# Kernel tuning notes

Hardware: AMD Instinct MI355X
Metric: run time of the kernel (lower is better)

Reference implementation:

```python
import jax, jax.numpy as jnp
import numpy as np

H_HEADS = 16
N_HID = 1024
D_K = N_HID // H_HEADS
EPS = 1e-6


def _linear(x, w, b):
    # torch nn.Linear: y = x @ W^T + b, W is [out, in]
    return jnp.einsum('bsi,oi->bso', x, w) + b


def _layernorm(x, a, b):
    # Faithful to custom LayerNorm: unbiased std (torch default) and (std + eps)
    mean = jnp.mean(x, axis=-1, keepdims=True)
    std = jnp.std(x, axis=-1, keepdims=True, ddof=1)
    return a * (x - mean) / (std + EPS) + b


def setup_inputs() -> dict:
    key = jax.random.key(0)
    ks = jax.random.split(key, 20)
    B, S, H = 4, 1024, N_HID
    s = 1.0 / np.sqrt(H)
    inp = {
        'x': jax.random.normal(ks[0], (B, S, H), dtype=jnp.float32),
        'mask': jax.random.randint(ks[1], (B, 1, 1, S), 0, 2, dtype=jnp.int32),
        'wq': jax.random.normal(ks[2], (H, H), dtype=jnp.float32) * s,
        'bq': jnp.zeros((H,), jnp.float32),
        'wk': jax.random.normal(ks[3], (H, H), dtype=jnp.float32) * s,
        'bk': jnp.zeros((H,), jnp.float32),
        'wv': jax.random.normal(ks[4], (H, H), dtype=jnp.float32) * s,
        'bv': jnp.zeros((H,), jnp.float32),
        'wo': jax.random.normal(ks[5], (H, H), dtype=jnp.float32) * s,
        'bo': jnp.zeros((H,), jnp.float32),
        'w1': jax.random.normal(ks[6], (2 * H, H), dtype=jnp.float32) * s,
        'b1': jnp.zeros((2 * H,), jnp.float32),
        'w2': jax.random.normal(ks[7], (H, 2 * H), dtype=jnp.float32) * (1.0 / np.sqrt(2 * H)),
        'b2': jnp.zeros((H,), jnp.float32),
        'g1': jnp.ones((H,), jnp.float32),
        'be1': jnp.zeros((H,), jnp.float32),
        'g2': jnp.ones((H,), jnp.float32),
        'be2': jnp.zeros((H,), jnp.float32),
    }
    return inp


def _forward(x, mask, wq, bq, wk, bk, wv, bv, wo, bo, w1, b1, w2, b2, g1, be1, g2, be2):
    B, S, H = x.shape
    # --- multi-head self-attention ---
    q = _linear(x, wq, bq).reshape(B, S, H_HEADS, D_K).transpose(0, 2, 1, 3)  # [B,h,S,dk]
    k = _linear(x, wk, bk).reshape(B, S, H_HEADS, D_K).transpose(0, 2, 1, 3)
    v = _linear(x, wv, bv).reshape(B, S, H_HEADS, D_K).transpose(0, 2, 1, 3)
    scores = jnp.einsum('bhqd,bhkd->bhqk', q, k) / np.sqrt(D_K)  # [B,h,S,S]
    scores = jnp.where(mask == 0, jnp.float32(-1e9), scores)
    p = jax.nn.softmax(scores, axis=-1)
    attn_out = jnp.einsum('bhqk,bhkd->bhqd', p, v)
    attn_out = attn_out.transpose(0, 2, 1, 3).reshape(B, S, H)
    attn_out = _linear(attn_out, wo, bo)
    # sublayer 0: residual + layernorm (dropout = identity at eval)
    x = _layernorm(x + attn_out, g1, be1)
    # --- positionwise FFN ---
    ff = _linear(jax.nn.relu(_linear(x, w1, b1)), w2, b2)
    # sublayer 1
    return _layernorm(x + ff, g2, be2)


def reference(x, mask, wq, bq, wk, bk, wv, bv, wo, bo, w1, b1, w2, b2, g1, be1, g2, be2):
    return _forward(x, mask, wq, bq, wk, bk, wv, bv, wo, bo, w1, b1, w2, b2, g1, be1, g2, be2)
```

## Files before the change

### kernel.cpp

```cpp
#include <hip/hip_runtime.h>

typedef __attribute__((ext_vector_type(8))) short short8;
typedef __attribute__((ext_vector_type(4))) float f32x4;
typedef __attribute__((ext_vector_type(4))) unsigned short us4;

#define LOG2E 1.4426950408889634f

__device__ __forceinline__ unsigned short f2bf(float f) {
  unsigned int u = __float_as_uint(f);
  u += 0x7FFFu + ((u >> 16) & 1u);
  return (unsigned short)(u >> 16);
}

__global__ __launch_bounds__(256) void cvt_all(
    const float* __restrict__ x, const float* __restrict__ wq, const float* __restrict__ wk,
    const float* __restrict__ wv, const float* __restrict__ wo, const float* __restrict__ w1,
    const float* __restrict__ w2,
    unsigned short* __restrict__ xb, unsigned short* __restrict__ wqkvb,
    unsigned short* __restrict__ wob, unsigned short* __restrict__ w1b,
    unsigned short* __restrict__ w2b) {
  int i = blockIdx.x * 256 + threadIdx.x;
  for (int t = i; t < 3145728; t += 786432) {
    const float* src; unsigned short* dst; int lo;
    if (t < 1048576)      { src = x;  dst = xb;              lo = t; }
    else if (t < 1310720) { src = wq; dst = wqkvb;           lo = t - 1048576; }
    else if (t < 1572864) { src = wk; dst = wqkvb + 1048576; lo = t - 1310720; }
    else if (t < 1835008) { src = wv; dst = wqkvb + 2097152; lo = t - 1572864; }
    else if (t < 2097152) { src = wo; dst = wob;             lo = t - 1835008; }
    else if (t < 2621440) { src = w1; dst = w1b;             lo = t - 2097152; }
    else                  { src = w2; dst = w2b;             lo = t - 2621440; }
    float4 v = ((const float4*)src)[lo];
    us4 o = { f2bf(v.x), f2bf(v.y), f2bf(v.z), f2bf(v.w) };
    *(us4*)(dst + (size_t)lo * 4) = o;
  }
}

#define GLL16(g, l) __builtin_amdgcn_global_load_lds( \
    (const __attribute__((address_space(1))) void*)(g), \
    (__attribute__((address_space(3))) void*)(l), 16, 0, 0)

template <int EPI>
__global__ __launch_bounds__(256) void gemm_bt(
    const unsigned short* __restrict__ A, const unsigned short* __restrict__ B,
    const float* __restrict__ bias, const float* __restrict__ res,
    void* __restrict__ out, int M, int N, int K) {
  __shared__ __align__(16) unsigned short As[128 * 64];
  __shared__ __align__(16) unsigned short Bs[128 * 64];
  const int tid = threadIdx.x;
  const int lane = tid & 63;
  const int w = tid >> 6;
  const int wr = w >> 1, wc = w & 1;
  const int l15 = lane & 15, l4 = lane >> 4;
  const int m0 = blockIdx.y * 128, n0 = blockIdx.x * 128;

  f32x4 acc[4][4] = {};

  const int nkt = K >> 6;
  for (int kt = 0; kt < nkt; ++kt) {
    __syncthreads();
#pragma unroll
    for (int i = 0; i < 4; ++i) {
      int c = (i * 4 + w) * 64 + lane;
      int row = c >> 3;
      int offb = (c & 7) * 16;
      int srcb = offb ^ ((row & 7) << 4);
      const unsigned short* ga = A + (size_t)(m0 + row) * K + kt * 64 + (srcb >> 1);
      GLL16(ga, As + (i * 4 + w) * 512);
      const unsigned short* gb = B + (size_t)(n0 + row) * K + kt * 64 + (srcb >> 1);
      GLL16(gb, Bs + (i * 4 + w) * 512);
    }
    __syncthreads();
#pragma unroll
    for (int ks = 0; ks < 2; ++ks) {
      short8 a[4], b[4];
#pragma unroll
      for (int mi = 0; mi < 4; ++mi) {
        int row = wr * 64 + mi * 16 + l15;
        int ke = (ks * 32 + l4 * 8) ^ ((row & 7) << 3);
        a[mi] = *(const short8*)(As + row * 64 + ke);
      }
#pragma unroll
      for (int ni = 0; ni < 4; ++ni) {
        int row = wc * 64 + ni * 16 + l15;
        int ke = (ks * 32 + l4 * 8) ^ ((row & 7) << 3);
        b[ni] = *(const short8*)(Bs + row * 64 + ke);
      }
#pragma unroll
      for (int mi = 0; mi < 4; ++mi)
#pragma unroll
        for (int ni = 0; ni < 4; ++ni)
          acc[mi][ni] = __builtin_amdgcn_mfma_f32_16x16x32_bf16(a[mi], b[ni], acc[mi][ni], 0, 0, 0);
    }
  }

#pragma unroll
  for (int mi = 0; mi < 4; ++mi) {
#pragma unroll
    for (int ni = 0; ni < 4; ++ni) {
      int n = n0 + wc * 64 + ni * 16 + l15;
      float bv = bias[n];
#pragma unroll
      for (int j = 0; j < 4; ++j) {
        int m = m0 + wr * 64 + mi * 16 + l4 * 4 + j;
        float v = acc[mi][ni][j] + bv;
        if (EPI == 0) {
          ((float*)out)[(size_t)m * N + n] = v + res[(size_t)m * N + n];
        } else {
          ((unsigned short*)out)[(size_t)m * N + n] = f2bf(v > 0.f ? v : 0.f);
        }
      }
    }
  }
}

template <int EPI>
__global__ __launch_bounds__(256) void gemm_bt64(
    const unsigned short* __restrict__ A, const unsigned short* __restrict__ B,
    const float* __restrict__ bias, const float* __restrict__ res,
    void* __restrict__ out, int M, int N, int K) {
  __shared__ __align__(16) unsigned short As[128 * 64];
  __shared__ __align__(16) unsigned short Bs[64 * 64];
  const int tid = threadIdx.x;
  const int lane = tid & 63;
  const int w = tid >> 6;
  const int l15 = lane & 15, l4 = lane >> 4;
  const int m0 = blockIdx.y * 128, n0 = blockIdx.x * 64;

  f32x4 acc[2][4] = {};

  const int nkt = K >> 6;
  for (int kt = 0; kt < nkt; ++kt) {
    __syncthreads();
#pragma unroll
    for (int i = 0; i < 4; ++i) {
      int chunk = i * 4 + w;
      int c = chunk * 64 + lane;
      int row = c >> 3;
      int offb = (c & 7) * 16;
      int srcb = offb ^ ((row & 7) << 4);
      GLL16(A + (size_t)(m0 + row) * K + kt * 64 + (srcb >> 1), As + chunk * 512);
    }
#pragma unroll
    for (int i = 0; i < 2; ++i) {
      int chunk = i * 4 + w;
      int c = chunk * 64 + lane;
      int row = c >> 3;
      int offb = (c & 7) * 16;
      int srcb = offb ^ ((row & 7) << 4);
      GLL16(B + (size_t)(n0 + row) * K + kt * 64 + (srcb >> 1), Bs + chunk * 512);
    }
    __syncthreads();
#pragma unroll
    for (int ks = 0; ks < 2; ++ks) {
      short8 a[2], b[4];
#pragma unroll
      for (int mi = 0; mi < 2; ++mi) {
        int row = w * 32 + mi * 16 + l15;
        int ke = (ks * 32 + l4 * 8) ^ ((row & 7) << 3);
        a[mi] = *(const short8*)(As + row * 64 + ke);
      }
#pragma unroll
      for (int ni = 0; ni < 4; ++ni) {
        int row = ni * 16 + l15;
        int ke = (ks * 32 + l4 * 8) ^ ((row & 7) << 3);
        b[ni] = *(const short8*)(Bs + row * 64 + ke);
      }
#pragma unroll
      for (int mi = 0; mi < 2; ++mi)
#pragma unroll
        for (int ni = 0; ni < 4; ++ni)
          acc[mi][ni] = __builtin_amdgcn_mfma_f32_16x16x32_bf16(a[mi], b[ni], acc[mi][ni], 0, 0, 0);
    }
  }

#pragma unroll
  for (int mi = 0; mi < 2; ++mi) {
#pragma unroll
    for (int ni = 0; ni < 4; ++ni) {
      int n = n0 + ni * 16 + l15;
      float bv = bias[n];
#pragma unroll
      for (int j = 0; j < 4; ++j) {
        int m = m0 + w * 32 + mi * 16 + l4 * 4 + j;
        float v = acc[mi][ni][j] + bv;
        if (EPI == 0) {
          ((float*)out)[(size_t)m * N + n] = v + res[(size_t)m * N + n];
        } else {
          ((unsigned short*)out)[(size_t)m * N + n] = f2bf(v > 0.f ? v : 0.f);
        }
      }
    }
  }
}

__global__ __launch_bounds__(256) void gemm_qkv(
    const unsigned short* __restrict__ A,
    const unsigned short* __restrict__ Bw,
    const float* __restrict__ bq, const float* __restrict__ bk, const float* __restrict__ bvv,
    unsigned short* __restrict__ Qo, unsigned short* __restrict__ Ko, unsigned short* __restrict__ Vto,
    int K) {
  __shared__ __align__(16) unsigned short As[128 * 64];
  __shared__ __align__(16) unsigned short Bs[128 * 64];
  const int tid = threadIdx.x;
  const int lane = tid & 63;
  const int w = tid >> 6;
  const int wr = w >> 1, wc = w & 1;
  const int l15 = lane & 15, l4 = lane >> 4;
  const int m0 = blockIdx.y * 128, n0 = blockIdx.x * 128;
  const bool swp = (n0 >= 2048);

  f32x4 acc[4][4] = {};

  const int nkt = K >> 6;
  for (int kt = 0; kt < nkt; ++kt) {
    __syncthreads();
#pragma unroll
    for (int i = 0; i < 4; ++i) {
      int c = (i * 4 + w) * 64 + lane;
      int row = c >> 3;
      int offb = (c & 7) * 16;
      int srcb = offb ^ ((row & 7) << 4);
      GLL16(A + (size_t)(m0 + row) * K + kt * 64 + (srcb >> 1), As + (i * 4 + w) * 512);
      GLL16(Bw + (size_t)(n0 + row) * K + kt * 64 + (srcb >> 1), Bs + (i * 4 + w) * 512);
    }
    __syncthreads();
#pragma unroll
    for (int ks = 0; ks < 2; ++ks) {
      short8 a[4], b[4];
#pragma unroll
      for (int mi = 0; mi < 4; ++mi) {
        int row = wr * 64 + mi * 16 + l15;
        int ke = (ks * 32 + l4 * 8) ^ ((row & 7) << 3);
        a[mi] = *(const short8*)(As + row * 64 + ke);
      }
#pragma unroll
      for (int ni = 0; ni < 4; ++ni) {
        int row = wc * 64 + ni * 16 + l15;
        int ke = (ks * 32 + l4 * 8) ^ ((row & 7) << 3);
        b[ni] = *(const short8*)(Bs + row * 64 + ke);
      }
      if (!swp) {
#pragma unroll
        for (int mi = 0; mi < 4; ++mi)
#pragma unroll
          for (int ni = 0; ni < 4; ++ni)
            acc[mi][ni] = __builtin_amdgcn_mfma_f32_16x16x32_bf16(a[mi], b[ni], acc[mi][ni], 0, 0, 0);
      } else {
#pragma unroll
        for (int mi = 0; mi < 4; ++mi)
#pragma unroll
          for (int ni = 0; ni < 4; ++ni)
            acc[mi][ni] = __builtin_amdgcn_mfma_f32_16x16x32_bf16(b[ni], a[mi], acc[mi][ni], 0, 0, 0);
      }
    }
  }

  if (!swp) {
#pragma unroll
    for (int mi = 0; mi < 4; ++mi) {
#pragma unroll
      for (int ni = 0; ni < 4; ++ni) {
        int n = n0 + wc * 64 + ni * 16 + l15;
        int seg = n >> 10;
        int nn = n & 1023;
        int h_ = nn >> 6, d_ = nn & 63;
        float bval = (seg == 0 ? bq : bk)[nn];
#pragma unroll
        for (int j = 0; j < 4; ++j) {
          int m = m0 + wr * 64 + mi * 16 + l4 * 4 + j;
          int b_ = m >> 10, s_ = m & 1023;
          float v = acc[mi][ni][j] + bval;
          size_t headbase = ((size_t)(b_ * 16 + h_)) << 16;
          if (seg == 0) Qo[headbase + (s_ << 6) + d_] = f2bf(v * 0.125f);
          else          Ko[headbase + (s_ << 6) + d_] = f2bf(v);
        }
      }
    }
  } else {
#pragma unroll
    for (int ni = 0; ni < 4; ++ni) {
      float bval[4];
      int nbase = (n0 & 1023) + wc * 64 + ni * 16 + l4 * 4;
#pragma unroll
      for (int j = 0; j < 4; ++j) bval[j] = bvv[nbase + j];
#pragma unroll
      for (int mi = 0; mi < 4; ++mi) {
        int m = m0 + wr * 64 + mi * 16 + l15;
        int b_ = m >> 10, s_ = m & 1023;
#pragma unroll
        for (int j = 0; j < 4; ++j) {
          int nn = nbase + j;
          int h_ = nn >> 6, d_ = nn & 63;
          float v = acc[mi][ni][j] + bval[j];
          Vto[(((size_t)(b_ * 16 + h_)) << 16) + (d_ << 10) + s_] = f2bf(v);
        }
      }
    }
  }
}

__global__ __launch_bounds__(256) void attn_kernel(
    const unsigned short* __restrict__ Qg, const unsigned short* __restrict__ Kg,
    const unsigned short* __restrict__ Vtg, const int* __restrict__ mask,
    unsigned short* __restrict__ Og) {
  __shared__ __align__(16) unsigned short Qs[64 * 64];
  __shared__ __align__(16) unsigned short Ks[64 * 64];
  __shared__ __align__(16) unsigned short Vs[64 * 64];
  __shared__ __align__(16) unsigned short Ps[4][16 * 64];
  __shared__ float mkadd[1024];

  const int tid = threadIdx.x, lane = tid & 63, w = tid >> 6;
  const int l15 = lane & 15, l4 = lane >> 4;
  const int bh = blockIdx.y;
  const int b = bh >> 4, h = bh & 15;
  const int s0 = blockIdx.x * 64;

  const unsigned short* Qbase = Qg + ((size_t)bh << 16);
  const unsigned short* Kbase = Kg + ((size_t)bh << 16);
  const unsigned short* Vbase = Vtg + ((size_t)bh << 16);

#pragma unroll
  for (int i = 0; i < 4; ++i)
    mkadd[i * 256 + tid] = (mask[b * 1024 + i * 256 + tid] == 0) ? -1e9f : 0.f;

#pragma unroll
  for (int i = 0; i < 2; ++i) {
    int c = i * 256 + tid;
    int row = c >> 3, off8 = (c & 7) * 8;
    short8 v = *(const short8*)(Qbase + (size_t)(s0 + row) * 64 + off8);
    *(short8*)(&Qs[row * 64 + (off8 ^ ((row & 7) << 3))]) = v;
  }

  f32x4 o[4] = {};
  float l_st[4] = {0.f, 0.f, 0.f, 0.f};

  for (int kv = 0; kv < 16; ++kv) {
    int kv0 = kv * 64;
    __syncthreads();
#pragma unroll
    for (int i = 0; i < 2; ++i) {
      int c = i * 256 + tid;
      int row = c >> 3, off8 = (c & 7) * 8;
      short8 kvv = *(const short8*)(Kbase + (size_t)(kv0 + row) * 64 + off8);
      *(short8*)(&Ks[row * 64 + (off8 ^ ((row & 7) << 3))]) = kvv;
      short8 vv = *(const short8*)(Vbase + (size_t)row * 1024 + kv0 + off8);
      *(short8*)(&Vs[row * 64 + (off8 ^ ((row & 7) << 3))]) = vv;
    }
    __syncthreads();

    f32x4 sc[4] = {};
#pragma unroll
    for (int ks = 0; ks < 2; ++ks) {
      short8 a, bb[4];
      {
        int row = w * 16 + l15;
        int ke = (ks * 32 + l4 * 8) ^ ((row & 7) << 3);
        a = *(const short8*)(Qs + row * 64 + ke);
      }
#pragma unroll
      for (int ni = 0; ni < 4; ++ni) {
        int row = ni * 16 + l15;
        int ke = (ks * 32 + l4 * 8) ^ ((row & 7) << 3);
        bb[ni] = *(const short8*)(Ks + row * 64 + ke);
      }
#pragma unroll
      for (int ni = 0; ni < 4; ++ni)
        sc[ni] = __builtin_amdgcn_mfma_f32_16x16x32_bf16(a, bb[ni], sc[ni], 0, 0, 0);
    }

#pragma unroll
    for (int j = 0; j < 4; ++j) {
      int r = l4 * 4 + j;
      float ps = 0.f;
#pragma unroll
      for (int ni = 0; ni < 4; ++ni) {
        int cc = ni * 16 + l15;
        float p = exp2f(fmaf(sc[ni][j], LOG2E, mkadd[kv0 + cc]));
        ps += p;
        Ps[w][r * 64 + (cc ^ ((r & 7) << 3))] = f2bf(p);
      }
      l_st[j] += ps;
    }

#pragma unroll
    for (int ks = 0; ks < 2; ++ks) {
      short8 a, bb[4];
      {
        int row = l15;
        int ke = (ks * 32 + l4 * 8) ^ ((row & 7) << 3);
        a = *(const short8*)(&Ps[w][row * 64 + ke]);
      }
#pragma unroll
      for (int dt = 0; dt < 4; ++dt) {
        int row = dt * 16 + l15;
        int ke = (ks * 32 + l4 * 8) ^ ((row & 7) << 3);
        bb[dt] = *(const short8*)(Vs + row * 64 + ke);
      }
#pragma unroll
      for (int dt = 0; dt < 4; ++dt)
        o[dt] = __builtin_amdgcn_mfma_f32_16x16x32_bf16(a, bb[dt], o[dt], 0, 0, 0);
    }
  }

#pragma unroll
  for (int j = 0; j < 4; ++j) {
#pragma unroll
    for (int off = 1; off < 16; off <<= 1) l_st[j] += __shfl_xor(l_st[j], off, 64);
  }

#pragma unroll
  for (int j = 0; j < 4; ++j) {
    float inv = 1.f / l_st[j];
    int s = s0 + w * 16 + l4 * 4 + j;
#pragma unroll
    for (int dt = 0; dt < 4; ++dt) {
      int d = dt * 16 + l15;
      Og[(((size_t)(b * 1024 + s)) << 10) + h * 64 + d] = f2bf(o[dt][j] * inv);
    }
  }
}

template <int WRITE_BF16>
__global__ __launch_bounds__(256) void ln_kernel(
    const float* __restrict__ z, const float* __restrict__ g, const float* __restrict__ be,
    float* __restrict__ outf, unsigned short* __restrict__ outb) {
  int row = blockIdx.x * 4 + (threadIdx.x >> 6);
  int lane = threadIdx.x & 63;
  const float4* zp = (const float4*)(z + (size_t)row * 1024);
  float4 v[4];
  float sum = 0.f, sq = 0.f;
#pragma unroll
  for (int k = 0; k < 4; ++k) {
    v[k] = zp[lane + k * 64];
    sum += v[k].x + v[k].y + v[k].z + v[k].w;
    sq += v[k].x * v[k].x + v[k].y * v[k].y + v[k].z * v[k].z + v[k].w * v[k].w;
  }
#pragma unroll
  for (int off = 1; off < 64; off <<= 1) {
    sum += __shfl_xor(sum, off, 64);
    sq += __shfl_xor(sq, off, 64);
  }
  float mean = sum * (1.f / 1024.f);
  float var = fmaxf((sq - sum * mean) * (1.f / 1023.f), 0.f);
  float r = 1.f / (sqrtf(var) + 1e-6f);
#pragma unroll
  for (int k = 0; k < 4; ++k) {
    int c = lane + k * 64;
    float4 gv = ((const float4*)g)[c];
    float4 bv = ((const float4*)be)[c];
    float4 y;
    y.x = (v[k].x - mean) * r * gv.x + bv.x;
    y.y = (v[k].y - mean) * r * gv.y + bv.y;
    y.z = (v[k].z - mean) * r * gv.z + bv.z;
    y.w = (v[k].w - mean) * r * gv.w + bv.w;
    ((float4*)(outf + (size_t)row * 1024))[c] = y;
    if (WRITE_BF16) {
      us4 ob = { f2bf(y.x), f2bf(y.y), f2bf(y.z), f2bf(y.w) };
      *(us4*)(outb + (size_t)row * 1024 + c * 4) = ob;
    }
  }
}

extern "C" void kernel_launch(void* const* d_in, const int* in_sizes, int n_in,
                              void* d_out, int out_size, void* d_ws, size_t ws_size,
                              hipStream_t stream) {
  (void)in_sizes; (void)n_in; (void)out_size; (void)ws_size;
  const float* x   = (const float*)d_in[0];
  const int*   msk = (const int*)d_in[1];
  const float* wq  = (const float*)d_in[2];
  const float* bq  = (const float*)d_in[3];
  const float* wk  = (const float*)d_in[4];
  const float* bk  = (const float*)d_in[5];
  const float* wv  = (const float*)d_in[6];
  const float* bv  = (const float*)d_in[7];
  const float* wo  = (const float*)d_in[8];
  const float* bo  = (const float*)d_in[9];
  const float* w1  = (const float*)d_in[10];
  const float* b1  = (const float*)d_in[11];
  const float* w2  = (const float*)d_in[12];
  const float* b2  = (const float*)d_in[13];
  const float* g1  = (const float*)d_in[14];
  const float* be1 = (const float*)d_in[15];
  const float* g2  = (const float*)d_in[16];
  const float* be2 = (const float*)d_in[17];
  float* out = (float*)d_out;

  char* ws = (char*)d_ws;
  const size_t MB = 1 << 20;
  unsigned short* xb    = (unsigned short*)(ws + 0 * MB);
  unsigned short* wqkvb = (unsigned short*)(ws + 8 * MB);
  unsigned short* wob   = (unsigned short*)(ws + 14 * MB);
  unsigned short* w1b   = (unsigned short*)(ws + 16 * MB);
  unsigned short* w2b   = (unsigned short*)(ws + 20 * MB);
  unsigned short* Qb    = (unsigned short*)(ws + 24 * MB);
  unsigned short* Kb    = (unsigned short*)(ws + 32 * MB);
  unsigned short* Vtb   = (unsigned short*)(ws + 40 * MB);
  unsigned short* attnb = (unsigned short*)(ws + 48 * MB);
  float* z1   = (float*)(ws + 56 * MB);
  float* x1f  = (float*)(ws + 72 * MB);
  unsigned short* x1b = (unsigned short*)(ws + 88 * MB);
  unsigned short* h1  = (unsigned short*)(ws + 24 * MB);
  float* z2 = (float*)(ws + 56 * MB);

  dim3 blk(256);

  cvt_all<<<3072, blk, 0, stream>>>(x, wq, wk, wv, wo, w1, w2, xb, wqkvb, wob, w1b, w2b);

  gemm_qkv<<<dim3(24, 32), blk, 0, stream>>>(xb, wqkvb, bq, bk, bv, Qb, Kb, Vtb, 1024);

  attn_kernel<<<dim3(16, 64), blk, 0, stream>>>(Qb, Kb, Vtb, msk, attnb);

  gemm_bt64<0><<<dim3(16, 32), blk, 0, stream>>>(attnb, wob, bo, x, (void*)z1, 4096, 1024, 1024);
  ln_kernel<1><<<1024, blk, 0, stream>>>(z1, g1, be1, x1f, x1b);

  gemm_bt<3><<<dim3(16, 32), blk, 0, stream>>>(x1b, w1b, b1, nullptr, (void*)h1, 4096, 2048, 1024);
  gemm_bt64<0><<<dim3(16, 32), blk, 0, stream>>>(h1, w2b, b2, x1f, (void*)z2, 4096, 1024, 2048);
  ln_kernel<0><<<1024, blk, 0, stream>>>(z2, g2, be2, out, nullptr);
}
```

Baseline: 193.6 us.

## Double-buffer LDS tiles in GEMMs and shrink QKV tile to 128x64

The GEMM kernels now use two LDS buffers and issue the global-to-LDS loads for the next K tile before computing on the current one, with a single barrier per iteration instead of two. The separate 128- and 64-wide GEMM kernels are merged into one template. The QKV projection switches from 128x128 to 128x64 tiles, doubling its grid to raise occupancy and wave count. The cost is doubled LDS per block, which may reduce how many blocks fit per CU.

After: 183.2 us. 5.4% less time.

```diff
diff --git a/kernel.cpp b/kernel.cpp
--- a/kernel.cpp
+++ b/kernel.cpp
@@ -39,69 +39,83 @@
     (const __attribute__((address_space(1))) void*)(g), \
     (__attribute__((address_space(3))) void*)(l), 16, 0, 0)
 
-template <int EPI>
-__global__ __launch_bounds__(256) void gemm_bt(
+template <int BN, int EPI>
+__global__ __launch_bounds__(256) void gemm2(
     const unsigned short* __restrict__ A, const unsigned short* __restrict__ B,
     const float* __restrict__ bias, const float* __restrict__ res,
     void* __restrict__ out, int M, int N, int K) {
-  __shared__ __align__(16) unsigned short As[128 * 64];
-  __shared__ __align__(16) unsigned short Bs[128 * 64];
+  __shared__ __align__(16) unsigned short As[2][128 * 64];
+  __shared__ __align__(16) unsigned short Bs[2][BN * 64];
   const int tid = threadIdx.x;
   const int lane = tid & 63;
   const int w = tid >> 6;
-  const int wr = w >> 1, wc = w & 1;
   const int l15 = lane & 15, l4 = lane >> 4;
-  const int m0 = blockIdx.y * 128, n0 = blockIdx.x * 128;
-
-  f32x4 acc[4][4] = {};
+  const int m0 = blockIdx.y * 128, n0 = blockIdx.x * BN;
+
+  constexpr int MI = (BN == 128) ? 4 : 2;
+  f32x4 acc[MI][4] = {};
+
+  auto STAGE = [&](int buf, int kt) {
+#pragma unroll
+    for (int i = 0; i < 4; ++i) {
+      int chunk = i * 4 + w;
+      int c = chunk * 64 + lane;
+      int row = c >> 3;
+      int srcb = ((c & 7) * 16) ^ ((row & 7) << 4);
+      GLL16(A + (size_t)(m0 + row) * K + kt * 64 + (srcb >> 1), &As[buf][chunk * 512]);
+    }
+#pragma unroll
+    for (int i = 0; i < BN / 32; ++i) {
+      int chunk = i * 4 + w;
+      int c = chunk * 64 + lane;
+      int row = c >> 3;
+      int srcb = ((c & 7) * 16) ^ ((row & 7) << 4);
+      GLL16(B + (size_t)(n0 + row) * K + kt * 64 + (srcb >> 1), &Bs[buf][chunk * 512]);
+    }
+  };
 
   const int nkt = K >> 6;
+  STAGE(0, 0);
+  __syncthreads();
+  int cur = 0;
   for (int kt = 0; kt < nkt; ++kt) {
-    __syncthreads();
-#pragma unroll
-    for (int i = 0; i < 4; ++i) {
-      int c = (i * 4 + w) * 64 + lane;
-      int row = c >> 3;
-      int offb = (c & 7) * 16;
-      int srcb = offb ^ ((row & 7) << 4);
-      const unsigned short* ga = A + (size_t)(m0 + row) * K + kt * 64 + (srcb >> 1);
-      GLL16(ga, As + (i * 4 + w) * 512);
-      const unsigned short* gb = B + (size_t)(n0 + row) * K + kt * 64 + (srcb >> 1);
-      GLL16(gb, Bs + (i * 4 + w) * 512);
-    }
-    __syncthreads();
+    if (kt + 1 < nkt) STAGE(cur ^ 1, kt + 1);
+    const unsigned short* as = As[cur];
+    const unsigned short* bs = Bs[cur];
 #pragma unroll
     for (int ks = 0; ks < 2; ++ks) {
-      short8 a[4], b[4];
-#pragma unroll
-      for (int mi = 0; mi < 4; ++mi) {
-        int row = wr * 64 + mi * 16 + l15;
-        int ke = (ks * 32 + l4 * 8) ^ ((row & 7) << 3);
-        a[mi] = *(const short8*)(As + row * 64 + ke);
+      short8 a[MI], b[4];
+#pragma unroll
+      for (int mi = 0; mi < MI; ++mi) {
+        int row = (BN == 128 ? ((w >> 1) * 64) : (w * 32)) + mi * 16 + l15;
+        int ke = (ks * 32 + l4 * 8) ^ ((row & 7) << 3);
+        a[mi] = *(const short8*)(as + row * 64 + ke);
       }
 #pragma unroll
       for (int ni = 0; ni < 4; ++ni) {
-        int row = wc * 64 + ni * 16 + l15;
-        int ke = (ks * 32 + l4 * 8) ^ ((row & 7) << 3);
-        b[ni] = *(const short8*)(Bs + row * 64 + ke);
-      }
-#pragma unroll
-      for (int mi = 0; mi < 4; ++mi)
+        int row = (BN == 128 ? ((w & 1) * 64) : 0) + ni * 16 + l15;
+        int ke = (ks * 32 + l4 * 8) ^ ((row & 7) << 3);
+        b[ni] = *(const short8*)(bs + row * 64 + ke);
+      }
+#pragma unroll
+      for (int mi = 0; mi < MI; ++mi)
 #pragma unroll
         for (int ni = 0; ni < 4; ++ni)
           acc[mi][ni] = __builtin_amdgcn_mfma_f32_16x16x32_bf16(a[mi], b[ni], acc[mi][ni], 0, 0, 0);
     }
-  }
-
-#pragma unroll
-  for (int mi = 0; mi < 4; ++mi) {
+    __syncthreads();
+    cur ^= 1;
+  }
+
+#pragma unroll
+  for (int mi = 0; mi < MI; ++mi) {
 #pragma unroll
     for (int ni = 0; ni < 4; ++ni) {
-      int n = n0 + wc * 64 + ni * 16 + l15;
+      int n = n0 + (BN == 128 ? ((w & 1) * 64) : 0) + ni * 16 + l15;
       float bv = bias[n];
 #pragma unroll
       for (int j = 0; j < 4; ++j) {
-        int m = m0 + wr * 64 + mi * 16 + l4 * 4 + j;
+        int m = m0 + (BN == 128 ? ((w >> 1) * 64) : (w * 32)) + mi * 16 + l4 * 4 + j;
         float v = acc[mi][ni][j] + bv;
         if (EPI == 0) {
           ((float*)out)[(size_t)m * N + n] = v + res[(size_t)m * N + n];
@@ -113,161 +127,96 @@
   }
 }
 
-template <int EPI>
-__global__ __launch_bounds__(256) void gemm_bt64(
-    const unsigned short* __restrict__ A, const unsigned short* __restrict__ B,
-    const float* __restrict__ bias, const float* __restrict__ res,
-    void* __restrict__ out, int M, int N, int K) {
-  __shared__ __align__(16) unsigned short As[128 * 64];
-  __shared__ __align__(16) unsigned short Bs[64 * 64];
-  const int tid = threadIdx.x;
-  const int lane = tid & 63;
-  const int w = tid >> 6;
-  const int l15 = lane & 15, l4 = lane >> 4;
-  const int m0 = blockIdx.y * 128, n0 = blockIdx.x * 64;
-
-  f32x4 acc[2][4] = {};
-
-  const int nkt = K >> 6;
-  for (int kt = 0; kt < nkt; ++kt) {
-    __syncthreads();
-#pragma unroll
-    for (int i = 0; i < 4; ++i) {
-      int chunk = i * 4 + w;
-      int c = chunk * 64 + lane;
-      int row = c >> 3;
-      int offb = (c & 7) * 16;
-      int srcb = offb ^ ((row & 7) << 4);
-      GLL16(A + (size_t)(m0 + row) * K + kt * 64 + (srcb >> 1), As + chunk * 512);
-    }
-#pragma unroll
-    for (int i = 0; i < 2; ++i) {
-      int chunk = i * 4 + w;
-      int c = chunk * 64 + lane;
-      int row = c >> 3;
-      int offb = (c & 7) * 16;
-      int srcb = offb ^ ((row & 7) << 4);
-      GLL16(B + (size_t)(n0 + row) * K + kt * 64 + (srcb >> 1), Bs + chunk * 512);
-    }
-    __syncthreads();
-#pragma unroll
-    for (int ks = 0; ks < 2; ++ks) {
-      short8 a[2], b[4];
-#pragma unroll
-      for (int mi = 0; mi < 2; ++mi) {
-        int row = w * 32 + mi * 16 + l15;
-        int ke = (ks * 32 + l4 * 8) ^ ((row & 7) << 3);
-        a[mi] = *(const short8*)(As + row * 64 + ke);
-      }
-#pragma unroll
-      for (int ni = 0; ni < 4; ++ni) {
-        int row = ni * 16 + l15;
-        int ke = (ks * 32 + l4 * 8) ^ ((row & 7) << 3);
-        b[ni] = *(const short8*)(Bs + row * 64 + ke);
-      }
-#pragma unroll
-      for (int mi = 0; mi < 2; ++mi)
-#pragma unroll
-        for (int ni = 0; ni < 4; ++ni)
-          acc[mi][ni] = __builtin_amdgcn_mfma_f32_16x16x32_bf16(a[mi], b[ni], acc[mi][ni], 0, 0, 0);
-    }
-  }
-
-#pragma unroll
-  for (int mi = 0; mi < 2; ++mi) {
-#pragma unroll
-    for (int ni = 0; ni < 4; ++ni) {
-      int n = n0 + ni * 16 + l15;
-      float bv = bias[n];
-#pragma unroll
-      for (int j = 0; j < 4; ++j) {
-        int m = m0 + w * 32 + mi * 16 + l4 * 4 + j;
-        float v = acc[mi][ni][j] + bv;
-        if (EPI == 0) {
-          ((float*)out)[(size_t)m * N + n] = v + res[(size_t)m * N + n];
-        } else {
-          ((unsigned short*)out)[(size_t)m * N + n] = f2bf(v > 0.f ? v : 0.f);
-        }
-      }
-    }
-  }
-}
-
 __global__ __launch_bounds__(256) void gemm_qkv(
     const unsigned short* __restrict__ A,
     const unsigned short* __restrict__ Bw,
     const float* __restrict__ bq, const float* __restrict__ bk, const float* __restrict__ bvv,
     unsigned short* __restrict__ Qo, unsigned short* __restrict__ Ko, unsigned short* __restrict__ Vto,
     int K) {
-  __shared__ __align__(16) unsigned short As[128 * 64];
-  __shared__ __align__(16) unsigned short Bs[128 * 64];
+  __shared__ __align__(16) unsigned short As[2][128 * 64];
+  __shared__ __align__(16) unsigned short Bs[2][64 * 64];
   const int tid = threadIdx.x;
   const int lane = tid & 63;
   const int w = tid >> 6;
-  const int wr = w >> 1, wc = w & 1;
   const int l15 = lane & 15, l4 = lane >> 4;
-  const int m0 = blockIdx.y * 128, n0 = blockIdx.x * 128;
+  const int m0 = blockIdx.y * 128, n0 = blockIdx.x * 64;
   const bool swp = (n0 >= 2048);
 
-  f32x4 acc[4][4] = {};
+  f32x4 acc[2][4] = {};
+
+  auto STAGE = [&](int buf, int kt) {
+#pragma unroll
+    for (int i = 0; i < 4; ++i) {
+      int chunk = i * 4 + w;
+      int c = chunk * 64 + lane;
+      int row = c >> 3;
+      int srcb = ((c & 7) * 16) ^ ((row & 7) << 4);
+      GLL16(A + (size_t)(m0 + row) * K + kt * 64 + (srcb >> 1), &As[buf][chunk * 512]);
+    }
+#pragma unroll
+    for (int i = 0; i < 2; ++i) {
+      int chunk = i * 4 + w;
+      int c = chunk * 64 + lane;
+      int row = c >> 3;
+      int srcb = ((c & 7) * 16) ^ ((row & 7) << 4);
+      GLL16(Bw + (size_t)(n0 + row) * K + kt * 64 + (srcb >> 1), &Bs[buf][chunk * 512]);
+    }
+  };
 
   const int nkt = K >> 6;
+  STAGE(0, 0);
+  __syncthreads();
+  int cur = 0;
   for (int kt = 0; kt < nkt; ++kt) {
-    __syncthreads();
-#pragma unroll
-    for (int i = 0; i < 4; ++i) {
-      int c = (i * 4 + w) * 64 + lane;
-      int row = c >> 3;
-      int offb = (c & 7) * 16;
-      int srcb = offb ^ ((row & 7) << 4);
-      GLL16(A + (size_t)(m0 + row) * K + kt * 64 + (srcb >> 1), As + (i * 4 + w) * 512);
-      GLL16(Bw + (size_t)(n0 + row) * K + kt * 64 + (srcb >> 1), Bs + (i * 4 + w) * 512);
-    }
-    __syncthreads();
+    if (kt + 1 < nkt) STAGE(cur ^ 1, kt + 1);
+    const unsigned short* as = As[cur];
+    const unsigned short* bs = Bs[cur];
 #pragma unroll
     for (int ks = 0; ks < 2; ++ks) {
-      short8 a[4], b[4];
-#pragma unroll
-      for (int mi = 0; mi < 4; ++mi) {
-        int row = wr * 64 + mi * 16 + l15;
-        int ke = (ks * 32 + l4 * 8) ^ ((row & 7) << 3);
-        a[mi] = *(const short8*)(As + row * 64 + ke);
+      short8 a[2], b[4];
+#pragma unroll
+      for (int mi = 0; mi < 2; ++mi) {
+        int row = w * 32 + mi * 16 + l15;
+        int ke = (ks * 32 + l4 * 8) ^ ((row & 7) << 3);
+        a[mi] = *(const short8*)(as + row * 64 + ke);
       }
 #pragma unroll
       for (int ni = 0; ni < 4; ++ni) {
-        int row = wc * 64 + ni * 16 + l15;
-        int ke = (ks * 32 + l4 * 8) ^ ((row & 7) << 3);
-        b[ni] = *(const short8*)(Bs + row * 64 + ke);
+        int row = ni * 16 + l15;
+        int ke = (ks * 32 + l4 * 8) ^ ((row & 7) << 3);
+        b[ni] = *(const short8*)(bs + row * 64 + ke);
       }
       if (!swp) {
 #pragma unroll
-        for (int mi = 0; mi < 4; ++mi)
+        for (int mi = 0; mi < 2; ++mi)
 #pragma unroll
           for (int ni = 0; ni < 4; ++ni)
             acc[mi][ni] = __builtin_amdgcn_mfma_f32_16x16x32_bf16(a[mi], b[ni], acc[mi][ni], 0, 0, 0);
       } else {
 #pragma unroll
-        for (int mi = 0; mi < 4; ++mi)
+        for (int mi = 0; mi < 2; ++mi)
 #pragma unroll
           for (int ni = 0; ni < 4; ++ni)
             acc[mi][ni] = __builtin_amdgcn_mfma_f32_16x16x32_bf16(b[ni], a[mi], acc[mi][ni], 0, 0, 0);
       }
     }
+    __syncthreads();
+    cur ^= 1;
   }
 
   if (!swp) {
 #pragma unroll
-    for (int mi = 0; mi < 4; ++mi) {
+    for (int mi = 0; mi < 2; ++mi) {
 #pragma unroll
       for (int ni = 0; ni < 4; ++ni) {
-        int n = n0 + wc * 64 + ni * 16 + l15;
+        int n = n0 + ni * 16 + l15;
         int seg = n >> 10;
         int nn = n & 1023;
         int h_ = nn >> 6, d_ = nn & 63;
         float bval = (seg == 0 ? bq : bk)[nn];
 #pragma unroll
         for (int j = 0; j < 4; ++j) {
-          int m = m0 + wr * 64 + mi * 16 + l4 * 4 + j;
+          int m = m0 + w * 32 + mi * 16 + l4 * 4 + j;
           int b_ = m >> 10, s_ = m & 1023;
           float v = acc[mi][ni][j] + bval;
           size_t headbase = ((size_t)(b_ * 16 + h_)) << 16;
@@ -280,12 +229,12 @@
 #pragma unroll
     for (int ni = 0; ni < 4; ++ni) {
       float bval[4];
-      int nbase = (n0 & 1023) + wc * 64 + ni * 16 + l4 * 4;
+      int nbase = (n0 & 1023) + ni * 16 + l4 * 4;
 #pragma unroll
       for (int j = 0; j < 4; ++j) bval[j] = bvv[nbase + j];
 #pragma unroll
-      for (int mi = 0; mi < 4; ++mi) {
-        int m = m0 + wr * 64 + mi * 16 + l15;
+      for (int mi = 0; mi < 2; ++mi) {
+        int m = m0 + w * 32 + mi * 16 + l15;
         int b_ = m >> 10, s_ = m & 1023;
 #pragma unroll
         for (int j = 0; j < 4; ++j) {
@@ -506,14 +455,14 @@
 
   cvt_all<<<3072, blk, 0, stream>>>(x, wq, wk, wv, wo, w1, w2, xb, wqkvb, wob, w1b, w2b);
 
-  gemm_qkv<<<dim3(24, 32), blk, 0, stream>>>(xb, wqkvb, bq, bk, bv, Qb, Kb, Vtb, 1024);
+  gemm_qkv<<<dim3(48, 32), blk, 0, stream>>>(xb, wqkvb, bq, bk, bv, Qb, Kb, Vtb, 1024);
 
   attn_kernel<<<dim3(16, 64), blk, 0, stream>>>(Qb, Kb, Vtb, msk, attnb);
 
-  gemm_bt64<0><<<dim3(16, 32), blk, 0, stream>>>(attnb, wob, bo, x, (void*)z1, 4096, 1024, 1024);
+  gemm2<64, 0><<<dim3(16, 32), blk, 0, stream>>>(attnb, wob, bo, x, (void*)z1, 4096, 1024, 1024);
   ln_kernel<1><<<1024, blk, 0, stream>>>(z1, g1, be1, x1f, x1b);
 
-  gemm_bt<3><<<dim3(16, 32), blk, 0, stream>>>(x1b, w1b, b1, nullptr, (void*)h1, 4096, 2048, 1024);
-  gemm_bt64<0><<<dim3(16, 32), blk, 0, stream>>>(h1, w2b, b2, x1f, (void*)z2, 4096, 1024, 2048);
+  gemm2<128, 3><<<dim3(16, 32), blk, 0, stream>>>(x1b, w1b, b1, nullptr, (void*)h1, 4096, 2048, 1024);
+  gemm2<64, 0><<<dim3(16, 32), blk, 0, stream>>>(h1, w2b, b2, x1f, (void*)z2, 4096, 1024, 2048);
   ln_kernel<0><<<1024, blk, 0, stream>>>(z2, g2, be2, out, nullptr);
 }
```
